# Kernel optimization log

Measured on AMD Instinct MI355X. Metric: run time of the kernel, lower is better.

Reference implementation:

```python
import jax, jax.numpy as jnp
import numpy as np

NUM_HEADS = 16

def setup_inputs() -> dict:
    key = jax.random.key(0)
    k1, k2, k3 = jax.random.split(key, 3)
    B, N, C = 4, 4096, 1024
    x = jax.random.normal(k1, (B, N, C), dtype=jnp.float32)
    # xavier-uniform-ish scaled init for the dense kernels
    w_qkv = jax.random.normal(k2, (C, 3 * C), dtype=jnp.float32) * (2.0 / (C + 3 * C)) ** 0.5
    w_proj = jax.random.normal(k3, (C, C), dtype=jnp.float32) * (1.0 / C) ** 0.5
    b_proj = jnp.zeros((C,), dtype=jnp.float32)
    return {"x": x, "w_qkv": w_qkv, "w_proj": w_proj, "b_proj": b_proj}

def reference(x, w_qkv, w_proj, b_proj):
    B, N, C = x.shape
    H = NUM_HEADS
    D = C // H
    # qkv projection: (B, N, 3C) -> (3, B, H, N, D)
    qkv = (x @ w_qkv).reshape(B, N, 3, H, D).transpose(2, 0, 3, 1, 4)
    q, k, v = qkv[0], qkv[1], qkv[2]
    # feature map: elu + 1 (positive features)
    q = jax.nn.elu(q) + 1.0
    k = jax.nn.elu(k) + 1.0
    # kv outer-product accumulation: (B, H, D, D)
    kv = jnp.einsum('bhnd,bhne->bhde', k, v)
    numerator = jnp.einsum('bhnd,bhde->bhne', q, kv)        # (B, H, N, D)
    sum_k = k.sum(axis=-2)                                   # (B, H, D)
    denominator = jnp.einsum('bhnd,bhd->bhn', q, sum_k)[..., None]  # (B, H, N, 1)
    y = numerator / denominator                              # (B, H, N, D)
    y = y.transpose(0, 2, 1, 3).reshape(B, N, C)             # merge heads
    out = y @ w_proj + b_proj
    return out
```

## Files before the change

kernel.cpp:

```cpp
#include <hip/hip_runtime.h>

typedef __bf16 bf16x8 __attribute__((ext_vector_type(8)));
typedef float f32x4 __attribute__((ext_vector_type(4)));

typedef const unsigned int __attribute__((address_space(1)))* gas_p;
typedef unsigned int __attribute__((address_space(3)))* las_p;

__device__ __forceinline__ void gload_lds16(const void* g, void* l) {
  __builtin_amdgcn_global_load_lds((gas_p)g, (las_p)l, 16, 0, 0);
}

__device__ __forceinline__ unsigned short f2bf(float f) {
  union { float f; unsigned int u; } x; x.f = f;
  unsigned int r = x.u + 0x7fffu + ((x.u >> 16) & 1u);
  return (unsigned short)(r >> 16);
}
__device__ __forceinline__ float elu1(float x) {
  return x > 0.f ? x + 1.f : __expf(x);
}
__device__ __forceinline__ f32x4 mfma16(bf16x8 a, bf16x8 b, f32x4 c) {
  return __builtin_amdgcn_mfma_f32_16x16x32_bf16(a, b, c, 0, 0, 0);
}

#define BAR() __builtin_amdgcn_s_barrier()
#define VMW8() asm volatile("s_waitcnt vmcnt(8)" ::: "memory")
#define VMW4() asm volatile("s_waitcnt vmcnt(4)" ::: "memory")
#define VMW0() asm volatile("s_waitcnt vmcnt(0)" ::: "memory")
#define LGKM0() do { asm volatile("s_waitcnt lgkmcnt(0)" ::: "memory"); \
                     __builtin_amdgcn_sched_barrier(0); } while (0)


__global__ __launch_bounds__(256) void k_cvt_x(const float* __restrict__ x,
                                               unsigned short* __restrict__ xb, int n) {
  int i = (blockIdx.x * 256 + threadIdx.x) * 4;
  const int stride = gridDim.x * 256 * 4;
  for (; i < n; i += stride) {
    float4 v = *(const float4*)(x + i);
    union { unsigned short u[4]; uint2 q; } pk;
    pk.u[0] = f2bf(v.x); pk.u[1] = f2bf(v.y); pk.u[2] = f2bf(v.z); pk.u[3] = f2bf(v.w);
    *(uint2*)(xb + i) = pk.q;
  }
}

__global__ __launch_bounds__(256) void k_cvt_t(const float* __restrict__ w,
                                               unsigned short* __restrict__ wT,
                                               int R, int Cc) {
  __shared__ float t[32][33];
  const int j0 = blockIdx.x * 32, i0 = blockIdx.y * 32;
  const int tx = threadIdx.x & 31, ty = threadIdx.x >> 5;
#pragma unroll
  for (int k = 0; k < 4; ++k)
    t[ty + 8 * k][tx] = w[(size_t)(i0 + ty + 8 * k) * Cc + j0 + tx];
  __syncthreads();
#pragma unroll
  for (int k = 0; k < 4; ++k)
    wT[(size_t)(j0 + ty + 8 * k) * R + i0 + tx] = f2bf(t[tx][ty + 8 * k]);
}


template <int EPI>
__global__ __launch_bounds__(512, 2) void k_gemm256(
    const unsigned short* __restrict__ A, const unsigned short* __restrict__ BT, int NBX,
    unsigned short* __restrict__ qb, unsigned short* __restrict__ kT,
    unsigned short* __restrict__ vT, const float* __restrict__ bias,
    float* __restrict__ out) {
  extern __shared__ unsigned short lds[];
  unsigned short* Asb = lds;
  unsigned short* Bsb = lds + 32768;

  const int tid = threadIdx.x, lane = tid & 63, wave = tid >> 6;
  const int wm = wave >> 2, wn = wave & 3;
  int bid = blockIdx.x;
  { const int cpx = (int)gridDim.x >> 3; bid = (bid & 7) * cpx + (bid >> 3); }
  const int bx = bid % NBX, by = bid / NBX;
  const size_t bm0 = (size_t)by << 8, bn0 = (size_t)bx << 8;

  const int srow = (wave << 4) + (lane >> 2);
  const int gscol = ((lane & 3) << 3) ^ (((srow >> 1) & 3) << 3);
  const unsigned short* Ag0 = A + (bm0 + srow) * 1024 + gscol;
  const unsigned short* Bg0 = BT + (bn0 + srow) * 1024 + gscol;
  const int lws = wave << 9;

  auto stageA = [&](int slot, int kt, int kh) {
    const unsigned short* g_ = Ag0 + (kt << 6) + (kh << 5);
    unsigned short* l_ = Asb + (slot << 13) + lws;
    gload_lds16(g_, l_);
    gload_lds16(g_ + 128 * 1024, l_ + 4096);
  };
  auto stageB = [&](int slot, int kt, int kh) {
    const unsigned short* g_ = Bg0 + (kt << 6) + (kh << 5);
    unsigned short* l_ = Bsb + (slot << 13) + lws;
    gload_lds16(g_, l_);
    gload_lds16(g_ + 128 * 1024, l_ + 4096);
  };

  const int q8 = ((lane >> 4) << 3) ^ (((lane >> 1) & 3) << 3);
  const int ar_base = (wm << 7) + (lane & 15);
  const int br_base = (wn << 6) + (lane & 15);

  f32x4 acc[8][4] = {};

  stageA(0, 0, 0); stageB(0, 0, 0);
  stageA(1, 0, 1); stageB(1, 0, 1);
  stageA(2, 1, 0); stageB(2, 1, 0);
  VMW8();
  BAR();

#pragma unroll
  for (int t = 0; t < 16; ++t) {
    const int s0 = (2 * t) & 3, s1 = (2 * t + 1) & 3;
    const int sA = (2 * t + 3) & 3, sB = (2 * t + 4) & 3;
    const int t1 = t + 1, t2 = t + 2;
    bf16x8 af[4], bfr[4];

#pragma unroll
    for (int mi = 0; mi < 4; ++mi)
      af[mi] = *(const bf16x8*)&Asb[(s0 << 13) + ((ar_base + mi * 16) << 5) + q8];
#pragma unroll
    for (int n = 0; n < 4; ++n)
      bfr[n] = *(const bf16x8*)&Bsb[(s0 << 13) + ((br_base + n * 16) << 5) + q8];
    if (t < 15) stageA(sA, t1, 1);
    LGKM0();
    BAR();
    __builtin_amdgcn_s_setprio(1);
#pragma unroll
    for (int mi = 0; mi < 4; ++mi)
#pragma unroll
      for (int n = 0; n < 4; ++n) acc[mi][n] = mfma16(af[mi], bfr[n], acc[mi][n]);
    __builtin_amdgcn_s_setprio(0);

#pragma unroll
    for (int mi = 0; mi < 4; ++mi)
      af[mi] = *(const bf16x8*)&Asb[(s0 << 13) + ((ar_base + 64 + mi * 16) << 5) + q8];
    if (t < 15) stageB(sA, t1, 1);
    if (t < 15) { VMW8(); } else { VMW4(); }
    LGKM0();
    BAR();
    __builtin_amdgcn_s_setprio(1);
#pragma unroll
    for (int mi = 0; mi < 4; ++mi)
#pragma unroll
      for (int n = 0; n < 4; ++n) acc[4 + mi][n] = mfma16(af[mi], bfr[n], acc[4 + mi][n]);
    __builtin_amdgcn_s_setprio(0);

#pragma unroll
    for (int mi = 0; mi < 4; ++mi)
      af[mi] = *(const bf16x8*)&Asb[(s1 << 13) + ((ar_base + mi * 16) << 5) + q8];
#pragma unroll
    for (int n = 0; n < 4; ++n)
      bfr[n] = *(const bf16x8*)&Bsb[(s1 << 13) + ((br_base + n * 16) << 5) + q8];
    if (t < 14) stageA(sB, t2, 0);
    LGKM0();
    BAR();
    __builtin_amdgcn_s_setprio(1);
#pragma unroll
    for (int mi = 0; mi < 4; ++mi)
#pragma unroll
      for (int n = 0; n < 4; ++n) acc[mi][n] = mfma16(af[mi], bfr[n], acc[mi][n]);
    __builtin_amdgcn_s_setprio(0);

#pragma unroll
    for (int mi = 0; mi < 4; ++mi)
      af[mi] = *(const bf16x8*)&Asb[(s1 << 13) + ((ar_base + 64 + mi * 16) << 5) + q8];
    if (t < 14) stageB(sB, t2, 0);
    if (t < 14) { VMW8(); } else if (t == 14) { VMW4(); }
    LGKM0();
    BAR();
    __builtin_amdgcn_s_setprio(1);
#pragma unroll
    for (int mi = 0; mi < 4; ++mi)
#pragma unroll
      for (int n = 0; n < 4; ++n) acc[4 + mi][n] = mfma16(af[mi], bfr[n], acc[4 + mi][n]);
    __builtin_amdgcn_s_setprio(0);
  }
  VMW0();

  const int rbase = (int)bm0 + (wm << 7) + ((lane >> 4) << 2);
  const int cbase = (int)bn0 + (wn << 6) + (lane & 15);
  if constexpr (EPI == 0) {
    const int reg3 = (int)(bn0 >> 10);
#pragma unroll
    for (int m = 0; m < 8; ++m) {
      const int rb = rbase + m * 16;
#pragma unroll
      for (int n = 0; n < 4; ++n) {
        const int col = cbase + n * 16;
        if (reg3 == 0) {
#pragma unroll
          for (int i = 0; i < 4; ++i)
            qb[(size_t)(rb + i) * 1024 + col] = f2bf(elu1(acc[m][n][i]));
        } else {
          const int jc = col & 1023, h = jc >> 6, d = jc & 63;
          const int b_ = rb >> 12, n_ = rb & 4095;
          union { unsigned short u[4]; uint2 q; } pk;
          if (reg3 == 1) {
#pragma unroll
            for (int i = 0; i < 4; ++i) pk.u[i] = f2bf(elu1(acc[m][n][i]));
          } else {
#pragma unroll
            for (int i = 0; i < 4; ++i) pk.u[i] = f2bf(acc[m][n][i]);
          }
          unsigned short* dst = (reg3 == 1) ? kT : vT;
          *(uint2*)(dst + ((size_t)((b_ * 16 + h) * 64 + d) * 4096 + n_)) = pk.q;
        }
      }
    }
  } else {
#pragma unroll
    for (int n = 0; n < 4; ++n) {
      const int col = cbase + n * 16;
      const float bc = bias[col];
#pragma unroll
      for (int m = 0; m < 8; ++m) {
        const int rb = rbase + m * 16;
#pragma unroll
        for (int i = 0; i < 4; ++i)
          out[(size_t)(rb + i) * 1024 + col] = acc[m][n][i] + bc;
      }
    }
  }
}


__global__ __launch_bounds__(256) void k_kvpart(const unsigned short* __restrict__ kT,
                                                const unsigned short* __restrict__ vT,
                                                float* __restrict__ kvp,
                                                float* __restrict__ sumkp) {
  __shared__ unsigned short Ks[64 * 64];
  __shared__ unsigned short Vs[64 * 64];
  const int blk = blockIdx.x;
  const int bh = blk >> 3, ch = blk & 7;
  const int tid = threadIdx.x, lane = tid & 63, wave = tid >> 6;
  const unsigned short* kb = kT + (size_t)bh * 64 * 4096;
  const unsigned short* vb = vT + (size_t)bh * 64 * 4096;
  const int n0 = ch * 512;
  const int lrow = lane >> 3;
  const int lcolz = (((lane & 7) ^ (lane >> 3)) << 3);
  f32x4 acc[5] = {};

  bf16x8 ones_frag;
  {
    unsigned short o = ((lane & 15) == 0) ? (unsigned short)0x3F80 : (unsigned short)0;
    union { unsigned short u[8]; bf16x8 v; } c;
#pragma unroll
    for (int i = 0; i < 8; ++i) c.u[i] = o;
    ones_frag = c.v;
  }

  const int rxor = (lane & 7) << 3;
  const int col0 = (((lane >> 4) << 3)) ^ rxor;
  const int col1 = ((32 + ((lane >> 4) << 3))) ^ rxor;

  for (int ks = 0; ks < 512; ks += 64) {
    __syncthreads();
#pragma unroll
    for (int i = 0; i < 2; ++i) {
      const int c = i * 4 + wave;
      gload_lds16(kb + (size_t)(c * 8 + lrow) * 4096 + n0 + ks + lcolz, &Ks[c * 512]);
      gload_lds16(vb + (size_t)(c * 8 + lrow) * 4096 + n0 + ks + lcolz, &Vs[c * 512]);
    }
    __syncthreads();
    const int ar = wave * 16 + (lane & 15);
#pragma unroll
    for (int kk = 0; kk < 2; ++kk) {
      const int co = kk ? col1 : col0;
      bf16x8 a = *(const bf16x8*)&Ks[ar * 64 + co];
#pragma unroll
      for (int n = 0; n < 4; ++n) {
        bf16x8 bv = *(const bf16x8*)&Vs[(n * 16 + (lane & 15)) * 64 + co];
        acc[n] = mfma16(a, bv, acc[n]);
      }
      acc[4] = mfma16(a, ones_frag, acc[4]);
    }
  }
  float* dst = kvp + (size_t)blk * 64 * 64;
  const int d0 = wave * 16 + ((lane >> 4) << 2);
#pragma unroll
  for (int n = 0; n < 4; ++n)
#pragma unroll
    for (int i = 0; i < 4; ++i)
      dst[(d0 + i) * 64 + n * 16 + (lane & 15)] = acc[n][i];
  if ((lane & 15) == 0) {
#pragma unroll
    for (int i = 0; i < 4; ++i) sumkp[(size_t)blk * 64 + d0 + i] = acc[4][i];
  }
}


__global__ __launch_bounds__(256) void k_kvred(const float* __restrict__ kvp,
                                               const float* __restrict__ sumkp,
                                               unsigned short* __restrict__ kvsk) {
  const int bh = blockIdx.x, tid = threadIdx.x;
  const float* src = kvp + (size_t)bh * 8 * 4096;
  unsigned short* dst = kvsk + (size_t)bh * 80 * 64;
#pragma unroll
  for (int it = 0; it < 16; ++it) {
    const int idx = tid + it * 256;
    const int e = idx >> 6, d = idx & 63;
    float s = 0.f;
#pragma unroll
    for (int c = 0; c < 8; ++c) s += src[c * 4096 + d * 64 + e];
    dst[idx] = f2bf(s);
  }
#pragma unroll
  for (int it = 0; it < 4; ++it) {
    const int idx = tid + it * 256;
    const int e2 = idx >> 6, d = idx & 63;
    float v = 0.f;
    if (e2 == 0) {
#pragma unroll
      for (int c = 0; c < 8; ++c) v += sumkp[(size_t)(bh * 8 + c) * 64 + d];
    }
    dst[64 * 64 + idx] = f2bf(v);
  }
}


__global__ __launch_bounds__(256) void k_numer(const unsigned short* __restrict__ qb,
                                               const unsigned short* __restrict__ kvsk,
                                               unsigned short* __restrict__ yb) {
  __shared__ unsigned short Bs[80 * 64];
  const int bh = blockIdx.y;
  const int b = bh >> 4, h = bh & 15;
  const int n0 = blockIdx.x << 7;
  const int tid = threadIdx.x, lane = tid & 63, wave = tid >> 6;
  {
    const uint4* src = (const uint4*)(kvsk + (size_t)bh * 80 * 64);
    uint4* dst = (uint4*)Bs;
    for (int i = tid; i < 640; i += 256) dst[i ^ ((i >> 3) & 7)] = src[i];
  }
  __syncthreads();

  const int ko = (lane >> 4) << 3;
  const int rx = (lane & 7) << 3;
  f32x4 acc[2][5] = {};
  const unsigned short* qrow =
      qb + (size_t)(b * 4096 + n0 + wave * 32 + (lane & 15)) * 1024 + h * 64;
#pragma unroll
  for (int kk = 0; kk < 2; ++kk) {
    bf16x8 a[2], bb[5];
#pragma unroll
    for (int m = 0; m < 2; ++m)
      a[m] = *(const bf16x8*)(qrow + (size_t)m * 16 * 1024 + ko + kk * 32);
#pragma unroll
    for (int n = 0; n < 5; ++n)
      bb[n] = *(const bf16x8*)&Bs[(n * 16 + (lane & 15)) * 64 + ((ko + kk * 32) ^ rx)];
#pragma unroll
    for (int m = 0; m < 2; ++m)
#pragma unroll
      for (int n = 0; n < 5; ++n)
        acc[m][n] = mfma16(a[m], bb[n], acc[m][n]);
  }

  const int rbase = b * 4096 + n0 + wave * 32 + ((lane >> 4) << 2);
#pragma unroll
  for (int m = 0; m < 2; ++m) {
    f32x4 inv;
#pragma unroll
    for (int i = 0; i < 4; ++i) {
      float den = __shfl(acc[m][4][i], lane & 48);
      inv[i] = __builtin_amdgcn_rcpf(den);
    }
#pragma unroll
    for (int n = 0; n < 4; ++n) {
      const int col = h * 64 + n * 16 + (lane & 15);
#pragma unroll
      for (int i = 0; i < 4; ++i)
        yb[(size_t)(rbase + m * 16 + i) * 1024 + col] = f2bf(acc[m][n][i] * inv[i]);
    }
  }
}


extern "C" void kernel_launch(void* const* d_in, const int* in_sizes, int n_in,
                              void* d_out, int out_size, void* d_ws, size_t ws_size,
                              hipStream_t stream) {
  const float* x = (const float*)d_in[0];
  const float* w_qkv = (const float*)d_in[1];
  const float* w_proj = (const float*)d_in[2];
  const float* b_proj = (const float*)d_in[3];
  float* out = (float*)d_out;
  char* ws = (char*)d_ws;

  unsigned short* xb = (unsigned short*)(ws);
  unsigned short* wqkvT = (unsigned short*)(ws + 33554432);
  unsigned short* wprojT = (unsigned short*)(ws + 39845888);
  unsigned short* qb = (unsigned short*)(ws + 41943040);
  unsigned short* kT = (unsigned short*)(ws + 75497472);
  unsigned short* vT = (unsigned short*)(ws + 109051904);
  float* kvp = (float*)(ws + 142606336);
  unsigned short* kvsk = (unsigned short*)(ws + 151011328);
  unsigned short* yb = xb;
  float* sumkp = (float*)wqkvT;

  k_cvt_x<<<2048, 256, 0, stream>>>(x, xb, 4 * 4096 * 1024);
  k_cvt_t<<<dim3(96, 32), 256, 0, stream>>>(w_qkv, wqkvT, 1024, 3072);
  k_cvt_t<<<dim3(32, 32), 256, 0, stream>>>(w_proj, wprojT, 1024, 1024);
  k_gemm256<0><<<768, 512, 131072, stream>>>(xb, wqkvT, 12, qb, kT, vT, nullptr, nullptr);
  k_kvpart<<<512, 256, 0, stream>>>(kT, vT, kvp, sumkp);
  k_kvred<<<64, 256, 0, stream>>>(kvp, sumkp, kvsk);
  k_numer<<<dim3(32, 64), 256, 0, stream>>>(qb, kvsk, yb);
  k_gemm256<1><<<256, 512, 131072, stream>>>(yb, wprojT, 4, nullptr, nullptr, nullptr,
                                             b_proj, out);
}
```

Measured before the change: 224.7 us.

## Split GEMM into QKV and projection kernels with double-buffered LDS

The templated 256x256 GEMM is split into two kernels. The QKV kernel moves from a four-slot, two-stage-ahead LDS pipeline to a two-slot double buffer, halving shared memory per block (128KB to 64KB) so two blocks can reside per CU. The projection kernel uses 128x256 tiles with 48KB of LDS and 512 blocks to fill the device better. In exchange, prefetch depth shrinks and each step now waits on vmcnt(0), which can expose global-load latency.

```diff
diff --git a/kernel.cpp b/kernel.cpp
--- a/kernel.cpp
+++ b/kernel.cpp
@@ -23,8 +23,6 @@
 }
 
 #define BAR() __builtin_amdgcn_s_barrier()
-#define VMW8() asm volatile("s_waitcnt vmcnt(8)" ::: "memory")
-#define VMW4() asm volatile("s_waitcnt vmcnt(4)" ::: "memory")
 #define VMW0() asm volatile("s_waitcnt vmcnt(0)" ::: "memory")
 #define LGKM0() do { asm volatile("s_waitcnt lgkmcnt(0)" ::: "memory"); \
                      __builtin_amdgcn_sched_barrier(0); } while (0)
@@ -58,21 +56,19 @@
 }
 
 
-template <int EPI>
-__global__ __launch_bounds__(512, 2) void k_gemm256(
-    const unsigned short* __restrict__ A, const unsigned short* __restrict__ BT, int NBX,
+__global__ __launch_bounds__(512, 2) void k_gemmq(
+    const unsigned short* __restrict__ A, const unsigned short* __restrict__ BT,
     unsigned short* __restrict__ qb, unsigned short* __restrict__ kT,
-    unsigned short* __restrict__ vT, const float* __restrict__ bias,
-    float* __restrict__ out) {
+    unsigned short* __restrict__ vT) {
   extern __shared__ unsigned short lds[];
   unsigned short* Asb = lds;
-  unsigned short* Bsb = lds + 32768;
+  unsigned short* Bsb = lds + 16384;
 
   const int tid = threadIdx.x, lane = tid & 63, wave = tid >> 6;
   const int wm = wave >> 2, wn = wave & 3;
   int bid = blockIdx.x;
   { const int cpx = (int)gridDim.x >> 3; bid = (bid & 7) * cpx + (bid >> 3); }
-  const int bx = bid % NBX, by = bid / NBX;
+  const int bx = bid % 12, by = bid / 12;
   const size_t bm0 = (size_t)by << 8, bn0 = (size_t)bx << 8;
 
   const int srow = (wave << 4) + (lane >> 2);
@@ -81,15 +77,15 @@
   const unsigned short* Bg0 = BT + (bn0 + srow) * 1024 + gscol;
   const int lws = wave << 9;
 
-  auto stageA = [&](int slot, int kt, int kh) {
-    const unsigned short* g_ = Ag0 + (kt << 6) + (kh << 5);
-    unsigned short* l_ = Asb + (slot << 13) + lws;
+  auto stageA = [&](int pair) {
+    const unsigned short* g_ = Ag0 + (pair << 5);
+    unsigned short* l_ = Asb + ((pair & 1) << 13) + lws;
     gload_lds16(g_, l_);
     gload_lds16(g_ + 128 * 1024, l_ + 4096);
   };
-  auto stageB = [&](int slot, int kt, int kh) {
-    const unsigned short* g_ = Bg0 + (kt << 6) + (kh << 5);
-    unsigned short* l_ = Bsb + (slot << 13) + lws;
+  auto stageB = [&](int pair) {
+    const unsigned short* g_ = Bg0 + (pair << 5);
+    unsigned short* l_ = Bsb + ((pair & 1) << 13) + lws;
     gload_lds16(g_, l_);
     gload_lds16(g_ + 128 * 1024, l_ + 4096);
   };
@@ -100,123 +96,150 @@
 
   f32x4 acc[8][4] = {};
 
-  stageA(0, 0, 0); stageB(0, 0, 0);
-  stageA(1, 0, 1); stageB(1, 0, 1);
-  stageA(2, 1, 0); stageB(2, 1, 0);
-  VMW8();
+  stageA(0); stageB(0);
+  VMW0();
   BAR();
 
-#pragma unroll
-  for (int t = 0; t < 16; ++t) {
-    const int s0 = (2 * t) & 3, s1 = (2 * t + 1) & 3;
-    const int sA = (2 * t + 3) & 3, sB = (2 * t + 4) & 3;
-    const int t1 = t + 1, t2 = t + 2;
-    bf16x8 af[4], bfr[4];
-
-#pragma unroll
-    for (int mi = 0; mi < 4; ++mi)
-      af[mi] = *(const bf16x8*)&Asb[(s0 << 13) + ((ar_base + mi * 16) << 5) + q8];
-#pragma unroll
-    for (int n = 0; n < 4; ++n)
-      bfr[n] = *(const bf16x8*)&Bsb[(s0 << 13) + ((br_base + n * 16) << 5) + q8];
-    if (t < 15) stageA(sA, t1, 1);
-    LGKM0();
-    BAR();
-    __builtin_amdgcn_s_setprio(1);
-#pragma unroll
-    for (int mi = 0; mi < 4; ++mi)
-#pragma unroll
-      for (int n = 0; n < 4; ++n) acc[mi][n] = mfma16(af[mi], bfr[n], acc[mi][n]);
-    __builtin_amdgcn_s_setprio(0);
-
-#pragma unroll
-    for (int mi = 0; mi < 4; ++mi)
-      af[mi] = *(const bf16x8*)&Asb[(s0 << 13) + ((ar_base + 64 + mi * 16) << 5) + q8];
-    if (t < 15) stageB(sA, t1, 1);
-    if (t < 15) { VMW8(); } else { VMW4(); }
-    LGKM0();
-    BAR();
-    __builtin_amdgcn_s_setprio(1);
-#pragma unroll
-    for (int mi = 0; mi < 4; ++mi)
-#pragma unroll
-      for (int n = 0; n < 4; ++n) acc[4 + mi][n] = mfma16(af[mi], bfr[n], acc[4 + mi][n]);
-    __builtin_amdgcn_s_setprio(0);
-
-#pragma unroll
-    for (int mi = 0; mi < 4; ++mi)
-      af[mi] = *(const bf16x8*)&Asb[(s1 << 13) + ((ar_base + mi * 16) << 5) + q8];
-#pragma unroll
-    for (int n = 0; n < 4; ++n)
-      bfr[n] = *(const bf16x8*)&Bsb[(s1 << 13) + ((br_base + n * 16) << 5) + q8];
-    if (t < 14) stageA(sB, t2, 0);
-    LGKM0();
-    BAR();
-    __builtin_amdgcn_s_setprio(1);
-#pragma unroll
-    for (int mi = 0; mi < 4; ++mi)
-#pragma unroll
-      for (int n = 0; n < 4; ++n) acc[mi][n] = mfma16(af[mi], bfr[n], acc[mi][n]);
-    __builtin_amdgcn_s_setprio(0);
-
-#pragma unroll
-    for (int mi = 0; mi < 4; ++mi)
-      af[mi] = *(const bf16x8*)&Asb[(s1 << 13) + ((ar_base + 64 + mi * 16) << 5) + q8];
-    if (t < 14) stageB(sB, t2, 0);
-    if (t < 14) { VMW8(); } else if (t == 14) { VMW4(); }
-    LGKM0();
-    BAR();
-    __builtin_amdgcn_s_setprio(1);
-#pragma unroll
-    for (int mi = 0; mi < 4; ++mi)
-#pragma unroll
-      for (int n = 0; n < 4; ++n) acc[4 + mi][n] = mfma16(af[mi], bfr[n], acc[4 + mi][n]);
-    __builtin_amdgcn_s_setprio(0);
-  }
-  VMW0();
+#define QKV_PAIR(P, SOFF)                                                             \
+  {                                                                                   \
+    bf16x8 af[4], bfr[4];                                                             \
+    _Pragma("unroll") for (int mi = 0; mi < 4; ++mi)                                  \
+        af[mi] = *(const bf16x8*)&Asb[(SOFF) + ((ar_base + mi * 16) << 5) + q8];      \
+    _Pragma("unroll") for (int n = 0; n < 4; ++n)                                     \
+        bfr[n] = *(const bf16x8*)&Bsb[(SOFF) + ((br_base + n * 16) << 5) + q8];       \
+    if ((P) < 31) { stageA((P) + 1); stageB((P) + 1); }                               \
+    LGKM0();                                                                          \
+    BAR();                                                                            \
+    __builtin_amdgcn_s_setprio(1);                                                    \
+    _Pragma("unroll") for (int mi = 0; mi < 4; ++mi)                                  \
+        _Pragma("unroll") for (int n = 0; n < 4; ++n)                                 \
+            acc[mi][n] = mfma16(af[mi], bfr[n], acc[mi][n]);                          \
+    __builtin_amdgcn_s_setprio(0);                                                    \
+    _Pragma("unroll") for (int mi = 0; mi < 4; ++mi)                                  \
+        af[mi] = *(const bf16x8*)&Asb[(SOFF) + ((ar_base + 64 + mi * 16) << 5) + q8]; \
+    VMW0();                                                                           \
+    LGKM0();                                                                          \
+    BAR();                                                                            \
+    __builtin_amdgcn_s_setprio(1);                                                    \
+    _Pragma("unroll") for (int mi = 0; mi < 4; ++mi)                                  \
+        _Pragma("unroll") for (int n = 0; n < 4; ++n)                                 \
+            acc[4 + mi][n] = mfma16(af[mi], bfr[n], acc[4 + mi][n]);                  \
+    __builtin_amdgcn_s_setprio(0);                                                    \
+  }
+
+  for (int p = 0; p < 32; p += 2) {
+    QKV_PAIR(p, 0)
+    QKV_PAIR(p + 1, 8192)
+  }
+#undef QKV_PAIR
 
   const int rbase = (int)bm0 + (wm << 7) + ((lane >> 4) << 2);
   const int cbase = (int)bn0 + (wn << 6) + (lane & 15);
-  if constexpr (EPI == 0) {
-    const int reg3 = (int)(bn0 >> 10);
-#pragma unroll
-    for (int m = 0; m < 8; ++m) {
-      const int rb = rbase + m * 16;
-#pragma unroll
-      for (int n = 0; n < 4; ++n) {
-        const int col = cbase + n * 16;
-        if (reg3 == 0) {
-#pragma unroll
-          for (int i = 0; i < 4; ++i)
-            qb[(size_t)(rb + i) * 1024 + col] = f2bf(elu1(acc[m][n][i]));
-        } else {
-          const int jc = col & 1023, h = jc >> 6, d = jc & 63;
-          const int b_ = rb >> 12, n_ = rb & 4095;
-          union { unsigned short u[4]; uint2 q; } pk;
-          if (reg3 == 1) {
-#pragma unroll
-            for (int i = 0; i < 4; ++i) pk.u[i] = f2bf(elu1(acc[m][n][i]));
-          } else {
-#pragma unroll
-            for (int i = 0; i < 4; ++i) pk.u[i] = f2bf(acc[m][n][i]);
-          }
-          unsigned short* dst = (reg3 == 1) ? kT : vT;
-          *(uint2*)(dst + ((size_t)((b_ * 16 + h) * 64 + d) * 4096 + n_)) = pk.q;
-        }
-      }
-    }
-  } else {
+  const int reg3 = (int)(bn0 >> 10);
+#pragma unroll
+  for (int m = 0; m < 8; ++m) {
+    const int rb = rbase + m * 16;
 #pragma unroll
     for (int n = 0; n < 4; ++n) {
       const int col = cbase + n * 16;
-      const float bc = bias[col];
-#pragma unroll
-      for (int m = 0; m < 8; ++m) {
-        const int rb = rbase + m * 16;
+      if (reg3 == 0) {
 #pragma unroll
         for (int i = 0; i < 4; ++i)
-          out[(size_t)(rb + i) * 1024 + col] = acc[m][n][i] + bc;
+          qb[(size_t)(rb + i) * 1024 + col] = f2bf(elu1(acc[m][n][i]));
+      } else {
+        const int jc = col & 1023, h = jc >> 6, d = jc & 63;
+        const int b_ = rb >> 12, n_ = rb & 4095;
+        union { unsigned short u[4]; uint2 q; } pk;
+        if (reg3 == 1) {
+#pragma unroll
+          for (int i = 0; i < 4; ++i) pk.u[i] = f2bf(elu1(acc[m][n][i]));
+        } else {
+#pragma unroll
+          for (int i = 0; i < 4; ++i) pk.u[i] = f2bf(acc[m][n][i]);
+        }
+        unsigned short* dst = (reg3 == 1) ? kT : vT;
+        *(uint2*)(dst + ((size_t)((b_ * 16 + h) * 64 + d) * 4096 + n_)) = pk.q;
       }
+    }
+  }
+}
+
+
+__global__ __launch_bounds__(512, 2) void k_gemmp(
+    const unsigned short* __restrict__ A, const unsigned short* __restrict__ BT,
+    const float* __restrict__ bias, float* __restrict__ out) {
+  extern __shared__ unsigned short lds[];
+  unsigned short* Asb = lds;
+  unsigned short* Bsb = lds + 8192;
+
+  const int tid = threadIdx.x, lane = tid & 63, wave = tid >> 6;
+  const int wm = wave >> 2, wn = wave & 3;
+  int bid = blockIdx.x;
+  { const int cpx = (int)gridDim.x >> 3; bid = (bid & 7) * cpx + (bid >> 3); }
+  const int bx = bid % 4, by = bid / 4;
+  const size_t bm0 = (size_t)by << 7, bn0 = (size_t)bx << 8;
+
+  const int srow = (wave << 4) + (lane >> 2);
+  const int gscol = ((lane & 3) << 3) ^ (((srow >> 1) & 3) << 3);
+  const unsigned short* Ag0 = A + (bm0 + srow) * 1024 + gscol;
+  const unsigned short* Bg0 = BT + (bn0 + srow) * 1024 + gscol;
+
+  auto stageA = [&](int pair) {
+    gload_lds16(Ag0 + (pair << 5), Asb + ((pair & 1) << 12) + (wave << 9));
+  };
+  auto stageB = [&](int pair) {
+    const unsigned short* g_ = Bg0 + (pair << 5);
+    unsigned short* l_ = Bsb + ((pair & 1) << 13) + (wave << 9);
+    gload_lds16(g_, l_);
+    gload_lds16(g_ + 128 * 1024, l_ + 4096);
+  };
+
+  const int q8 = ((lane >> 4) << 3) ^ (((lane >> 1) & 3) << 3);
+  const int ar_base = (wm << 6) + (lane & 15);
+  const int br_base = (wn << 6) + (lane & 15);
+
+  f32x4 acc[4][4] = {};
+
+  stageA(0); stageB(0);
+  VMW0();
+  BAR();
+
+#define PRJ_PAIR(P, SA, SB)                                                           \
+  {                                                                                   \
+    bf16x8 af[4], bfr[4];                                                             \
+    _Pragma("unroll") for (int mi = 0; mi < 4; ++mi)                                  \
+        af[mi] = *(const bf16x8*)&Asb[(SA) + ((ar_base + mi * 16) << 5) + q8];        \
+    _Pragma("unroll") for (int n = 0; n < 4; ++n)                                     \
+        bfr[n] = *(const bf16x8*)&Bsb[(SB) + ((br_base + n * 16) << 5) + q8];         \
+    if ((P) < 31) { stageA((P) + 1); stageB((P) + 1); }                               \
+    VMW0();                                                                           \
+    LGKM0();                                                                          \
+    BAR();                                                                            \
+    __builtin_amdgcn_s_setprio(1);                                                    \
+    _Pragma("unroll") for (int mi = 0; mi < 4; ++mi)                                  \
+        _Pragma("unroll") for (int n = 0; n < 4; ++n)                                 \
+            acc[mi][n] = mfma16(af[mi], bfr[n], acc[mi][n]);                          \
+    __builtin_amdgcn_s_setprio(0);                                                    \
+  }
+
+  for (int p = 0; p < 32; p += 2) {
+    PRJ_PAIR(p, 0, 0)
+    PRJ_PAIR(p + 1, 4096, 8192)
+  }
+#undef PRJ_PAIR
+
+  const int rbase = (int)bm0 + (wm << 6) + ((lane >> 4) << 2);
+  const int cbase = (int)bn0 + (wn << 6) + (lane & 15);
+#pragma unroll
+  for (int n = 0; n < 4; ++n) {
+    const int col = cbase + n * 16;
+    const float bc = bias[col];
+#pragma unroll
+    for (int m = 0; m < 4; ++m) {
+      const int rb = rbase + m * 16;
+#pragma unroll
+      for (int i = 0; i < 4; ++i)
+        out[(size_t)(rb + i) * 1024 + col] = acc[m][n][i] + bc;
     }
   }
 }
@@ -396,10 +419,9 @@
   k_cvt_x<<<2048, 256, 0, stream>>>(x, xb, 4 * 4096 * 1024);
   k_cvt_t<<<dim3(96, 32), 256, 0, stream>>>(w_qkv, wqkvT, 1024, 3072);
   k_cvt_t<<<dim3(32, 32), 256, 0, stream>>>(w_proj, wprojT, 1024, 1024);
-  k_gemm256<0><<<768, 512, 131072, stream>>>(xb, wqkvT, 12, qb, kT, vT, nullptr, nullptr);
+  k_gemmq<<<768, 512, 65536, stream>>>(xb, wqkvT, qb, kT, vT);
   k_kvpart<<<512, 256, 0, stream>>>(kT, vT, kvp, sumkp);
   k_kvred<<<64, 256, 0, stream>>>(kvp, sumkp, kvsk);
   k_numer<<<dim3(32, 64), 256, 0, stream>>>(qb, kvsk, yb);
-  k_gemm256<1><<<256, 512, 131072, stream>>>(yb, wprojT, 4, nullptr, nullptr, nullptr,
-                                             b_proj, out);
-}
+  k_gemmp<<<512, 512, 49152, stream>>>(yb, wprojT, b_proj, out);
+}
```

After: 227.0 us. About the same (+1.0%).
